# Kernel tuning notes

Hardware: AMD Instinct MI355X
Metric: run time of the kernel (lower is better)

Reference implementation:

```python
import jax, jax.numpy as jnp
from jax import lax
import numpy as np

B, S, D, H = 8, 1024, 512, 8
DH, FF, INNER, K = D // H, 4 * D, 2 * D, 31
SQRT_D = float(np.sqrt(D))  # module scales by sqrt(dim), not sqrt(dim_head)


def _ln(x, g, b, eps=1e-5):
    m = jnp.mean(x, -1, keepdims=True)
    v = jnp.var(x, -1, keepdims=True)
    return (x - m) / jnp.sqrt(v + eps) * g + b


def _swish(x):
    return x * jax.nn.sigmoid(x)


def _ff(x, g, b, w1, b1, w2, b2):
    return _swish(_ln(x, g, b) @ w1 + b1) @ w2 + b2


def _pos_encoding(s, d):
    pos = jnp.arange(s, dtype=jnp.float32)[:, None]
    div = jnp.exp(jnp.arange(0, d, 2, dtype=jnp.float32) * (-np.log(10000.0) / d))
    pe = jnp.zeros((s, d), jnp.float32)
    pe = pe.at[:, 0::2].set(jnp.sin(pos * div))
    pe = pe.at[:, 1::2].set(jnp.cos(pos * div))
    return pe


def _rel_shift(ps):  # (b, h, s, t) Transformer-XL relative shift
    b, h, s, t = ps.shape
    ps = jnp.pad(ps, ((0, 0), (0, 0), (0, 0), (1, 0)))
    return ps.reshape(b, h, t + 1, s)[:, :, 1:].reshape(b, h, s, t)


def _forward(x, ff1_ln_g, ff1_ln_b, ff1_w1, ff1_b1, ff1_w2, ff1_b2,
             attn_ln_g, attn_ln_b, wq, bq, wk, bk, wv, bv, wpos,
             u_bias, v_bias, wo, bo,
             conv_ln_g, conv_ln_b, pw1_w, pw1_b, dw_w, dw_b,
             bn_g, bn_b, bn_mean, bn_var, pw2_w, pw2_b,
             ff2_ln_g, ff2_ln_b, ff2_w1, ff2_b1, ff2_w2, ff2_b2,
             norm_g, norm_b):
    b, s, d = x.shape
    # FF1 half-residual
    x = 0.5 * _ff(x, ff1_ln_g, ff1_ln_b, ff1_w1, ff1_b1, ff1_w2, ff1_b2) + x
    # relative-position multi-head self-attention
    y = _ln(x, attn_ln_g, attn_ln_b)
    q = (y @ wq + bq).reshape(b, s, H, DH)
    k = (y @ wk + bk).reshape(b, s, H, DH)
    v = (y @ wv + bv).reshape(b, s, H, DH)
    pos = (_pos_encoding(s, d) @ wpos).reshape(s, H, DH)  # identical across batch
    score = jnp.einsum('bshd,bthd->bhst', q + u_bias, k)
    pos_score = _rel_shift(jnp.einsum('bshd,thd->bhst', q + v_bias, pos))
    attn = jax.nn.softmax((score + pos_score) / SQRT_D, axis=-1)
    ctx = jnp.einsum('bhst,bthd->bshd', attn, v).reshape(b, s, d)
    x = ctx @ wo + bo + x
    # conformer conv module: LN -> pointwise -> GLU -> depthwise -> BN -> swish -> pointwise
    c = _ln(x, conv_ln_g, conv_ln_b) @ pw1_w + pw1_b  # (b, s, 2*inner)
    a, gate = jnp.split(c, 2, axis=-1)
    z = jnp.transpose(a * jax.nn.sigmoid(gate), (0, 2, 1))  # (b, inner, s)
    z = jnp.pad(z, ((0, 0), (0, 0), (K // 2, K // 2)))  # pad (15, 15) for k=31
    z = lax.conv_general_dilated(z, dw_w[:, None, :], (1,), 'VALID',
                                 dimension_numbers=('NCH', 'OIH', 'NCH'),
                                 feature_group_count=INNER) + dw_b[None, :, None]
    z = (z - bn_mean[None, :, None]) * (bn_g / jnp.sqrt(bn_var + 1e-5))[None, :, None] + bn_b[None, :, None]
    z = _swish(z)
    x = jnp.transpose(z, (0, 2, 1)) @ pw2_w + pw2_b + x
    # FF2 half-residual + final LN
    x = 0.5 * _ff(x, ff2_ln_g, ff2_ln_b, ff2_w1, ff2_b1, ff2_w2, ff2_b2) + x
    return _ln(x, norm_g, norm_b)


def setup_inputs() -> dict:
    key = jax.random.key(0)
    ks = iter(jax.random.split(key, 64))

    def w(shape, scale=0.02):
        return scale * jax.random.normal(next(ks), shape, jnp.float32)

    return {
        'x': jax.random.normal(next(ks), (B, S, D), jnp.float32),
        'ff1_ln_g': jnp.ones(D, jnp.float32), 'ff1_ln_b': jnp.zeros(D, jnp.float32),
        'ff1_w1': w((D, FF)), 'ff1_b1': jnp.zeros(FF, jnp.float32),
        'ff1_w2': w((FF, D)), 'ff1_b2': jnp.zeros(D, jnp.float32),
        'attn_ln_g': jnp.ones(D, jnp.float32), 'attn_ln_b': jnp.zeros(D, jnp.float32),
        'wq': w((D, D)), 'bq': jnp.zeros(D, jnp.float32),
        'wk': w((D, D)), 'bk': jnp.zeros(D, jnp.float32),
        'wv': w((D, D)), 'bv': jnp.zeros(D, jnp.float32),
        'wpos': w((D, D)),
        'u_bias': w((H, DH)), 'v_bias': w((H, DH)),
        'wo': w((D, D)), 'bo': jnp.zeros(D, jnp.float32),
        'conv_ln_g': jnp.ones(D, jnp.float32), 'conv_ln_b': jnp.zeros(D, jnp.float32),
        'pw1_w': w((D, 2 * INNER)), 'pw1_b': jnp.zeros(2 * INNER, jnp.float32),
        'dw_w': w((INNER, K)), 'dw_b': jnp.zeros(INNER, jnp.float32),
        'bn_g': jnp.ones(INNER, jnp.float32), 'bn_b': jnp.zeros(INNER, jnp.float32),
        'bn_mean': jnp.zeros(INNER, jnp.float32), 'bn_var': jnp.ones(INNER, jnp.float32),
        'pw2_w': w((INNER, D)), 'pw2_b': jnp.zeros(D, jnp.float32),
        'ff2_ln_g': jnp.ones(D, jnp.float32), 'ff2_ln_b': jnp.zeros(D, jnp.float32),
        'ff2_w1': w((D, FF)), 'ff2_b1': jnp.zeros(FF, jnp.float32),
        'ff2_w2': w((FF, D)), 'ff2_b2': jnp.zeros(D, jnp.float32),
        'norm_g': jnp.ones(D, jnp.float32), 'norm_b': jnp.zeros(D, jnp.float32),
    }


def reference(x, ff1_ln_g, ff1_ln_b, ff1_w1, ff1_b1, ff1_w2, ff1_b2,
              attn_ln_g, attn_ln_b, wq, bq, wk, bk, wv, bv, wpos,
              u_bias, v_bias, wo, bo,
              conv_ln_g, conv_ln_b, pw1_w, pw1_b, dw_w, dw_b,
              bn_g, bn_b, bn_mean, bn_var, pw2_w, pw2_b,
              ff2_ln_g, ff2_ln_b, ff2_w1, ff2_b1, ff2_w2, ff2_b2,
              norm_g, norm_b):
    return _forward(x, ff1_ln_g, ff1_ln_b, ff1_w1, ff1_b1, ff1_w2, ff1_b2,
                    attn_ln_g, attn_ln_b, wq, bq, wk, bk, wv, bv, wpos,
                    u_bias, v_bias, wo, bo,
                    conv_ln_g, conv_ln_b, pw1_w, pw1_b, dw_w, dw_b,
                    bn_g, bn_b, bn_mean, bn_var, pw2_w, pw2_b,
                    ff2_ln_g, ff2_ln_b, ff2_w1, ff2_b1, ff2_w2, ff2_b2,
                    norm_g, norm_b)
```

## Files before the change

kernel.cpp:

```cpp
#include <hip/hip_runtime.h>
#include <cstdint>
#include <cstddef>

#define B_ 8
#define S_ 1024
#define D_ 512
#define H_ 8
#define DH_ 64
#define FF_ 2048
#define INNER_ 1024
#define NROWS 8192
#define INV_SQRT_D 0.04419417382415922f

typedef __attribute__((ext_vector_type(8))) short bf16x8;
typedef __attribute__((ext_vector_type(4))) float f32x4;
struct alignas(8) short4x { short x, y, z, w; };

__device__ __forceinline__ float sigmoidf_(float x) { return 1.f / (1.f + expf(-x)); }

__device__ __forceinline__ short f2bf(float f) {
  uint32_t u = __float_as_uint(f);
  u += 0x7fff + ((u >> 16) & 1);
  return (short)(u >> 16);
}
__device__ __forceinline__ float bf2f(short s) {
  return __uint_as_float(((uint32_t)(uint16_t)s) << 16);
}

__device__ __forceinline__ void store_out(float* C, size_t i, float v) { C[i] = v; }
__device__ __forceinline__ void store_out(short* C, size_t i, float v) { C[i] = f2bf(v); }

__device__ __forceinline__ void gload_lds16(const void* g, void* lds) {
  __builtin_amdgcn_global_load_lds(
      (const __attribute__((address_space(1))) uint32_t*)g,
      (__attribute__((address_space(3))) uint32_t*)lds, 16, 0, 0);
}

template <typename OutT>
__global__ __launch_bounds__(256) void ln_kernel(const float* __restrict__ in,
    const float* __restrict__ g, const float* __restrict__ b,
    OutT* __restrict__ out) {
  int row = blockIdx.x;
  const float* x = in + (size_t)row * D_;
  OutT* o = out + (size_t)row * D_;
  int t = threadIdx.x;
  float v0 = x[t], v1 = x[t + 256];
  float s = v0 + v1, q = v0 * v0 + v1 * v1;
#pragma unroll
  for (int off = 32; off > 0; off >>= 1) {
    s += __shfl_down(s, off);
    q += __shfl_down(q, off);
  }
  __shared__ float red[8];
  int wid = t >> 6, lane = t & 63;
  if (lane == 0) { red[wid] = s; red[wid + 4] = q; }
  __syncthreads();
  if (t == 0) {
    float S = red[0] + red[1] + red[2] + red[3];
    float Q = red[4] + red[5] + red[6] + red[7];
    float mean = S * (1.f / D_);
    float var = Q * (1.f / D_) - mean * mean;
    red[0] = mean;
    red[1] = rsqrtf(var + 1e-5f);
  }
  __syncthreads();
  float mean = red[0], inv = red[1];
  store_out(o, t, (v0 - mean) * inv * g[t] + b[t]);
  store_out(o, t + 256, (v1 - mean) * inv * g[t + 256] + b[t + 256]);
}

__global__ __launch_bounds__(256) void transpose_bf16_kernel(const float* __restrict__ in,
    short* __restrict__ out, int K, int N) {
  __shared__ float t[32][33];
  int n0 = blockIdx.x << 5, k0 = blockIdx.y << 5;
  int tx = threadIdx.x & 31, ty = threadIdx.x >> 5;
#pragma unroll
  for (int e = 0; e < 4; ++e)
    t[ty + e * 8][tx] = in[(size_t)(k0 + ty + e * 8) * N + n0 + tx];
  __syncthreads();
#pragma unroll
  for (int e = 0; e < 4; ++e)
    out[(size_t)(n0 + ty + e * 8) * K + k0 + tx] = f2bf(t[tx][ty + e * 8]);
}

template <int EPI, typename OutT>
__global__ __launch_bounds__(256) void mfma_gemm(const short* __restrict__ A,
    const short* __restrict__ Bt, const float* __restrict__ bias,
    const float* __restrict__ res, OutT* __restrict__ C, short* __restrict__ C2,
    const float* __restrict__ bias2, const float* __restrict__ bias3,
    int M, int N, int K) {
  __shared__ short As[128 * 32];
  __shared__ short Bs[128 * 32];
  int tid = threadIdx.x;
  int w = tid >> 6, l = tid & 63;
  int nwg = gridDim.x * gridDim.y;
  int flat = blockIdx.y * gridDim.x + blockIdx.x;
  int W = (flat & 7) * (nwg >> 3) + (flat >> 3);
  int bm = (W / gridDim.x) << 7, bn = (W % gridDim.x) << 7;
  int wr = w >> 1, wc = w & 1;
  f32x4 acc[4][4] = {};

  int sr = l >> 2, sc = l & 3;
  int r0 = (w * 2 + 0) * 16 + sr;
  int r1 = (w * 2 + 1) * 16 + sr;
  int g0 = sc ^ ((r0 >> 1) & 3);
  int g1 = sc ^ ((r1 >> 1) & 3);
  const short* a0 = A + (size_t)(bm + r0) * K + g0 * 8;
  const short* a1 = A + (size_t)(bm + r1) * K + g1 * 8;
  const short* b0 = Bt + (size_t)(bn + r0) * K + g0 * 8;
  const short* b1 = Bt + (size_t)(bn + r1) * K + g1 * 8;
  short* asd0 = As + (w * 2 + 0) * 512;
  short* asd1 = As + (w * 2 + 1) * 512;
  short* bsd0 = Bs + (w * 2 + 0) * 512;
  short* bsd1 = Bs + (w * 2 + 1) * 512;

  int lcol = l & 15, lk = l >> 4;
  int aoff[4], boff[4];
#pragma unroll
  for (int m = 0; m < 4; ++m) {
    int r = wr * 64 + m * 16 + lcol;
    aoff[m] = r * 32 + ((lk ^ ((r >> 1) & 3)) << 3);
  }
#pragma unroll
  for (int n = 0; n < 4; ++n) {
    int r = wc * 64 + n * 16 + lcol;
    boff[n] = r * 32 + ((lk ^ ((r >> 1) & 3)) << 3);
  }

  for (int k0 = 0; k0 < K; k0 += 32) {
    gload_lds16(a0 + k0, asd0);
    gload_lds16(a1 + k0, asd1);
    gload_lds16(b0 + k0, bsd0);
    gload_lds16(b1 + k0, bsd1);
    __syncthreads();
    bf16x8 af[4], bfr[4];
#pragma unroll
    for (int m = 0; m < 4; ++m) af[m] = *(const bf16x8*)(As + aoff[m]);
#pragma unroll
    for (int n = 0; n < 4; ++n) bfr[n] = *(const bf16x8*)(Bs + boff[n]);
#pragma unroll
    for (int m = 0; m < 4; ++m)
#pragma unroll
      for (int n = 0; n < 4; ++n)
        acc[m][n] = __builtin_amdgcn_mfma_f32_16x16x32_bf16(af[m], bfr[n], acc[m][n], 0, 0, 0);
    __syncthreads();
  }

  int lrow = (l >> 4) << 2;
#pragma unroll
  for (int m = 0; m < 4; ++m) {
    int row0 = bm + wr * 64 + m * 16 + lrow;
#pragma unroll
    for (int n = 0; n < 4; ++n) {
      int col = bn + wc * 64 + n * 16 + lcol;
      float bv = bias ? bias[col] : 0.f;
      if (EPI == 5) {
        short4x o;
        o.x = f2bf(acc[m][n][0] + bv);
        o.y = f2bf(acc[m][n][1] + bv);
        o.z = f2bf(acc[m][n][2] + bv);
        o.w = f2bf(acc[m][n][3] + bv);
        size_t tidx = ((size_t)(row0 >> 10) * 512 + col) * 1024 + (row0 & 1023);
        *(short4x*)((short*)C + tidx) = o;
      } else if (EPI == 4) {
#pragma unroll
        for (int r = 0; r < 4; ++r) {
          size_t idx = (size_t)(row0 + r) * N + col;
          float v = acc[m][n][r] + bv;
          ((short*)C)[idx] = f2bf(v + bias2[col]);
          C2[idx] = f2bf(v + bias3[col]);
        }
      } else {
#pragma unroll
        for (int r = 0; r < 4; ++r) {
          size_t idx = (size_t)(row0 + r) * N + col;
          float v = acc[m][n][r] + bv;
          if (EPI == 1) v = v * sigmoidf_(v);
          else if (EPI == 2) v = 0.5f * v + res[idx];
          else if (EPI == 3) v = v + res[idx];
          store_out(C, idx, v);
        }
      }
    }
  }
}

__global__ __launch_bounds__(256) void pe_kernel(short* __restrict__ pe) {
  int t = blockIdx.x, i = threadIdx.x;
  float freq = expf((float)(2 * i) * (-9.2103403719761836f / 512.f));
  float arg = (float)t * freq;
  pe[(size_t)t * D_ + 2 * i] = f2bf(sinf(arg));
  pe[(size_t)t * D_ + 2 * i + 1] = f2bf(cosf(arg));
}

__global__ __launch_bounds__(256) void attn_pos_mfma(const short* __restrict__ Qb,
    const short* __restrict__ Pos, short* __restrict__ Out, int bh0) {
  __shared__ short Qs[128 * 64];
  __shared__ short Ks[128 * 64];
  int tid = threadIdx.x;
  int w = tid >> 6, l = tid & 63;
  int z = blockIdx.z;
  int bh = bh0 + z, b = bh >> 3, h = bh & 7;
  int bi = blockIdx.y << 7, bj = blockIdx.x << 7;
  int srow = w * 8 + (l >> 3);
  int sch = l & 7;
#pragma unroll
  for (int cc = 0; cc < 4; ++cc) {
    int r = cc * 32 + srow;
    int g = sch ^ (r & 7);
    gload_lds16(Qb + (size_t)(b * S_ + bi + r) * D_ + h * DH_ + g * 8, Qs + (cc * 32 + w * 8) * 64);
    gload_lds16(Pos + (size_t)(bj + r) * D_ + h * DH_ + g * 8, Ks + (cc * 32 + w * 8) * 64);
  }
  __syncthreads();
  int wr = w >> 1, wc = w & 1;
  int lcol = l & 15, lk = l >> 4;
  bf16x8 qf[4][2], kf[4][2];
#pragma unroll
  for (int m = 0; m < 4; ++m)
#pragma unroll
    for (int ks = 0; ks < 2; ++ks) {
      int r = wr * 64 + m * 16 + lcol;
      int c = ks * 4 + lk;
      qf[m][ks] = *(const bf16x8*)(Qs + r * 64 + ((c ^ (r & 7)) << 3));
    }
#pragma unroll
  for (int n = 0; n < 4; ++n)
#pragma unroll
    for (int ks = 0; ks < 2; ++ks) {
      int r = wc * 64 + n * 16 + lcol;
      int c = ks * 4 + lk;
      kf[n][ks] = *(const bf16x8*)(Ks + r * 64 + ((c ^ (r & 7)) << 3));
    }
  f32x4 acc[4][4] = {};
#pragma unroll
  for (int ks = 0; ks < 2; ++ks)
#pragma unroll
    for (int m = 0; m < 4; ++m)
#pragma unroll
      for (int n = 0; n < 4; ++n)
        acc[m][n] = __builtin_amdgcn_mfma_f32_16x16x32_bf16(qf[m][ks], kf[n][ks], acc[m][n], 0, 0, 0);
  int lrow = (l >> 4) << 2;
  short* Oz = Out + (size_t)z * S_ * S_;
#pragma unroll
  for (int m = 0; m < 4; ++m)
#pragma unroll
    for (int r = 0; r < 4; ++r) {
      int iG = bi + wr * 64 + m * 16 + lrow + r;
#pragma unroll
      for (int n = 0; n < 4; ++n) {
        int tG = bj + wc * 64 + n * 16 + lcol;
        short val = f2bf(acc[m][n][r]);
        if (tG >= S_ - 1 - iG)
          Oz[(size_t)iG * S_ + (tG - (S_ - 1 - iG))] = val;
        else if (iG >= 1)
          Oz[(size_t)(iG - 1) * S_ + (tG + iG + 1)] = val;
        if (tG == 0 && iG < S_ - 1)
          Oz[(size_t)iG * S_ + iG + 1] = 0;
      }
    }
}

__global__ __launch_bounds__(512) void attn_fused(const short* __restrict__ qu,
    const short* __restrict__ kk, const short* __restrict__ vT,
    const short* __restrict__ Psh, short* __restrict__ ctx, int bh0) {
  __shared__ short Ks[2][64 * 64];
  __shared__ short Vs[2][64 * 64];
  __shared__ short Ps[128 * 64];
  int tid = threadIdx.x;
  int w = tid >> 6, l = tid & 63;
  int z = blockIdx.y;
  int bh = bh0 + z, b = bh >> 3, h = bh & 7;
  int i0 = blockIdx.x << 7;
  bf16x8 qf0, qf1;
  {
    const short* qrow = qu + (size_t)(b * S_ + i0 + w * 16 + (l & 15)) * D_ + h * DH_ + ((l >> 4) << 3);
    qf0 = *(const bf16x8*)(qrow);
    qf1 = *(const bf16x8*)(qrow + 32);
  }
  f32x4 po[4] = {};
  float mrow[4], lrw[4];
  int gi[4];
#pragma unroll
  for (int r = 0; r < 4; ++r) {
    mrow[r] = -1e30f;
    lrw[r] = 0.f;
    gi[r] = i0 + w * 16 + ((l >> 4) << 2) + r;
  }
  const short* prow0 = Psh + (size_t)z * S_ * S_ + (size_t)gi[0] * S_ + (l & 15);
  const short* prow1 = prow0 + S_;
  const short* prow2 = prow1 + S_;
  const short* prow3 = prow2 + S_;

  int srw = (w << 3) + (l >> 3);
  int sg = (l & 7) ^ (srw & 7);
  const short* ksrc = kk + (size_t)(b * S_) * D_ + h * DH_ + (sg << 3);
  const short* vsrc = vT + (size_t)(b * 512 + h * DH_ + srw) * 1024 + (sg << 3);
  int sdst = (w << 3) * 64;

#define STAGE_KV(jt, buf)                                                  \
  {                                                                        \
    int j0_ = (jt) << 6;                                                   \
    gload_lds16(ksrc + (size_t)(j0_ + srw) * D_, &Ks[buf][sdst]);          \
    gload_lds16(vsrc + j0_, &Vs[buf][sdst]);                               \
  }

  float pvc[4][4], pvn[4][4];
#define PLOADF(jt, dst)                                                    \
  {                                                                        \
    int j0_ = (jt) << 6;                                                   \
    _Pragma("unroll") for (int n_ = 0; n_ < 4; ++n_) {                     \
      dst[n_][0] = bf2f(prow0[j0_ + (n_ << 4)]);                           \
      dst[n_][1] = bf2f(prow1[j0_ + (n_ << 4)]);                           \
      dst[n_][2] = bf2f(prow2[j0_ + (n_ << 4)]);                           \
      dst[n_][3] = bf2f(prow3[j0_ + (n_ << 4)]);                           \
    }                                                                      \
  }

  STAGE_KV(0, 0);
  PLOADF(0, pvc);
  __syncthreads();

  for (int jt = 0; jt < 16; ++jt) {
    int buf = jt & 1;
    if (jt < 15) {
      STAGE_KV(jt + 1, buf ^ 1);
      PLOADF(jt + 1, pvn);
    }
    f32x4 sc[4] = {};
#pragma unroll
    for (int ks = 0; ks < 2; ++ks)
#pragma unroll
      for (int n = 0; n < 4; ++n) {
        int rj = (n << 4) + (l & 15);
        int ck = (ks << 2) + (l >> 4);
        bf16x8 kf = *(const bf16x8*)(&Ks[buf][rj * 64 + ((ck ^ (rj & 7)) << 3)]);
        sc[n] = __builtin_amdgcn_mfma_f32_16x16x32_bf16(ks == 0 ? qf0 : qf1, kf, sc[n], 0, 0, 0);
      }
    float pm[4];
#pragma unroll
    for (int r = 0; r < 4; ++r) pm[r] = -1e30f;
#pragma unroll
    for (int n = 0; n < 4; ++n)
#pragma unroll
      for (int r = 0; r < 4; ++r) {
        float v = (sc[n][r] + pvc[n][r]) * INV_SQRT_D;
        sc[n][r] = v;
        pm[r] = fmaxf(pm[r], v);
      }
#pragma unroll
    for (int r = 0; r < 4; ++r)
#pragma unroll
      for (int off = 1; off < 16; off <<= 1) pm[r] = fmaxf(pm[r], __shfl_xor(pm[r], off));
    float psum[4];
#pragma unroll
    for (int r = 0; r < 4; ++r) {
      float mn = fmaxf(mrow[r], pm[r]);
      float f = __expf(mrow[r] - mn);
      mrow[r] = mn;
      lrw[r] *= f;
#pragma unroll
      for (int n = 0; n < 4; ++n) po[n][r] *= f;
      psum[r] = 0.f;
    }
#pragma unroll
    for (int n = 0; n < 4; ++n)
#pragma unroll
      for (int r = 0; r < 4; ++r) {
        float p = __expf(sc[n][r] - mrow[r]);
        psum[r] += p;
        int rr = (w << 4) + ((l >> 4) << 2) + r;
        int c = (n << 4) + (l & 15);
        Ps[rr * 64 + (((c >> 3) ^ (rr & 7)) << 3) + (c & 7)] = f2bf(p);
      }
#pragma unroll
    for (int r = 0; r < 4; ++r) {
#pragma unroll
      for (int off = 1; off < 16; off <<= 1) psum[r] += __shfl_xor(psum[r], off);
      lrw[r] += psum[r];
    }
    int rr2 = (w << 4) + (l & 15);
    bf16x8 pa[2];
#pragma unroll
    for (int ks = 0; ks < 2; ++ks) {
      int ck = (ks << 2) + (l >> 4);
      pa[ks] = *(const bf16x8*)(&Ps[rr2 * 64 + ((ck ^ (rr2 & 7)) << 3)]);
    }
#pragma unroll
    for (int ks = 0; ks < 2; ++ks)
#pragma unroll
      for (int n = 0; n < 4; ++n) {
        int rd = (n << 4) + (l & 15);
        int ck = (ks << 2) + (l >> 4);
        bf16x8 vf = *(const bf16x8*)(&Vs[buf][rd * 64 + ((ck ^ (rd & 7)) << 3)]);
        po[n] = __builtin_amdgcn_mfma_f32_16x16x32_bf16(pa[ks], vf, po[n], 0, 0, 0);
      }
    __syncthreads();
    if (jt < 15) {
#pragma unroll
      for (int n = 0; n < 4; ++n)
#pragma unroll
        for (int r = 0; r < 4; ++r) pvc[n][r] = pvn[n][r];
    }
  }
  short* Cz = ctx + (size_t)b * S_ * D_ + h * DH_;
#pragma unroll
  for (int r = 0; r < 4; ++r) {
    float inv = 1.f / lrw[r];
#pragma unroll
    for (int n = 0; n < 4; ++n)
      Cz[(size_t)gi[r] * D_ + (n << 4) + (l & 15)] = f2bf(po[n][r] * inv);
  }
#undef STAGE_KV
#undef PLOADF
}

__global__ __launch_bounds__(256) void glu_kernel(const short* __restrict__ hbuf,
                                                  short* __restrict__ z) {
  size_t idx4 = ((size_t)blockIdx.x * 256 + threadIdx.x) << 2;
  size_t row = idx4 >> 10, c = idx4 & 1023;
  short4x a4 = *(const short4x*)(hbuf + row * 2048 + c);
  short4x g4 = *(const short4x*)(hbuf + row * 2048 + 1024 + c);
  short4x o;
  o.x = f2bf(bf2f(a4.x) * sigmoidf_(bf2f(g4.x)));
  o.y = f2bf(bf2f(a4.y) * sigmoidf_(bf2f(g4.y)));
  o.z = f2bf(bf2f(a4.z) * sigmoidf_(bf2f(g4.z)));
  o.w = f2bf(bf2f(a4.w) * sigmoidf_(bf2f(g4.w)));
  *(short4x*)(z + idx4) = o;
}

#define CTS 32
__global__ __launch_bounds__(256) void dwconv_kernel(const short* __restrict__ z,
    const float* __restrict__ w, const float* __restrict__ wb,
    const float* __restrict__ bng, const float* __restrict__ bnb,
    const float* __restrict__ bnm, const float* __restrict__ bnv,
    short* __restrict__ out) {
  int c = (blockIdx.z << 8) + threadIdx.x;
  int b = blockIdx.y;
  int s0 = blockIdx.x * CTS;
  float wr[31];
#pragma unroll
  for (int kk = 0; kk < 31; ++kk) wr[kk] = w[c * 31 + kk];
  float zv[CTS + 30];
#pragma unroll
  for (int e = 0; e < CTS + 30; ++e) {
    int sr = s0 - 15 + e;
    zv[e] = (sr >= 0 && sr < S_) ? bf2f(z[((size_t)(b * S_ + sr) << 10) + c]) : 0.f;
  }
  float scale = bng[c] * rsqrtf(bnv[c] + 1e-5f);
  float shift = bnb[c] - bnm[c] * scale;
  float bias = wb[c];
#pragma unroll
  for (int s = 0; s < CTS; ++s) {
    float acc = 0.f;
#pragma unroll
    for (int kk = 0; kk < 31; ++kk) acc += zv[s + kk] * wr[kk];
    float v = (acc + bias) * scale + shift;
    v = v * sigmoidf_(v);
    out[((size_t)(b * S_ + s0 + s) << 10) + c] = f2bf(v);
  }
}

extern "C" void kernel_launch(void* const* d_in, const int* in_sizes, int n_in,
                              void* d_out, int out_size, void* d_ws, size_t ws_size,
                              hipStream_t stream) {
  const float* x_in = (const float*)d_in[0];
  const float* ff1_ln_g = (const float*)d_in[1];
  const float* ff1_ln_b = (const float*)d_in[2];
  const float* ff1_w1 = (const float*)d_in[3];
  const float* ff1_b1 = (const float*)d_in[4];
  const float* ff1_w2 = (const float*)d_in[5];
  const float* ff1_b2 = (const float*)d_in[6];
  const float* attn_ln_g = (const float*)d_in[7];
  const float* attn_ln_b = (const float*)d_in[8];
  const float* wq = (const float*)d_in[9];
  const float* bq = (const float*)d_in[10];
  const float* wk = (const float*)d_in[11];
  const float* bk = (const float*)d_in[12];
  const float* wv = (const float*)d_in[13];
  const float* bv = (const float*)d_in[14];
  const float* wpos = (const float*)d_in[15];
  const float* u_bias = (const float*)d_in[16];
  const float* v_bias = (const float*)d_in[17];
  const float* wo = (const float*)d_in[18];
  const float* bo = (const float*)d_in[19];
  const float* conv_ln_g = (const float*)d_in[20];
  const float* conv_ln_b = (const float*)d_in[21];
  const float* pw1_w = (const float*)d_in[22];
  const float* pw1_b = (const float*)d_in[23];
  const float* dw_w = (const float*)d_in[24];
  const float* dw_b = (const float*)d_in[25];
  const float* bn_g = (const float*)d_in[26];
  const float* bn_b = (const float*)d_in[27];
  const float* bn_mean = (const float*)d_in[28];
  const float* bn_var = (const float*)d_in[29];
  const float* pw2_w = (const float*)d_in[30];
  const float* pw2_b = (const float*)d_in[31];
  const float* ff2_ln_g = (const float*)d_in[32];
  const float* ff2_ln_b = (const float*)d_in[33];
  const float* ff2_w1 = (const float*)d_in[34];
  const float* ff2_b1 = (const float*)d_in[35];
  const float* ff2_w2 = (const float*)d_in[36];
  const float* ff2_b2 = (const float*)d_in[37];
  const float* norm_g = (const float*)d_in[38];
  const float* norm_b = (const float*)d_in[39];

  char* wsb = (char*)d_ws;
  float* xb = (float*)(wsb);
  short* yb16 = (short*)(wsb + (16ull << 20));
  short* qu16 = (short*)(wsb + (24ull << 20));
  short* qv16 = (short*)(wsb + (32ull << 20));
  short* k16 = (short*)(wsb + (40ull << 20));
  short* vT16 = (short*)(wsb + (48ull << 20));
  short* ctx16 = (short*)(wsb + (56ull << 20));
  short* pos16 = (short*)(wsb + (64ull << 20));
  short* wt = (short*)(wsb + (65ull << 20));
  short* Pb16 = (short*)(wsb + (80ull << 20));
  short* hb16 = (short*)(wsb + (80ull << 20));
  short* zb16 = (short*)(wsb + (112ull << 20));
  short* cb16 = (short*)(wsb + (128ull << 20));
  short* peb16 = ctx16;

  short* ff1w1t = wt;
  short* ff1w2t = ff1w1t + 2048 * 512;
  short* wqt = ff1w2t + 512 * 2048;
  short* wkt = wqt + 512 * 512;
  short* wvt = wkt + 512 * 512;
  short* wot = wvt + 512 * 512;
  short* wpost = wot + 512 * 512;
  short* pw1t = wpost + 512 * 512;
  short* pw2t = pw1t + 2048 * 512;
  short* ff2w1t = pw2t + 512 * 1024;
  short* ff2w2t = ff2w1t + 2048 * 512;

  dim3 blk(256);

  transpose_bf16_kernel<<<dim3(64, 16), blk, 0, stream>>>(ff1_w1, ff1w1t, 512, 2048);
  transpose_bf16_kernel<<<dim3(16, 64), blk, 0, stream>>>(ff1_w2, ff1w2t, 2048, 512);
  transpose_bf16_kernel<<<dim3(16, 16), blk, 0, stream>>>(wq, wqt, 512, 512);
  transpose_bf16_kernel<<<dim3(16, 16), blk, 0, stream>>>(wk, wkt, 512, 512);
  transpose_bf16_kernel<<<dim3(16, 16), blk, 0, stream>>>(wv, wvt, 512, 512);
  transpose_bf16_kernel<<<dim3(16, 16), blk, 0, stream>>>(wo, wot, 512, 512);
  transpose_bf16_kernel<<<dim3(16, 16), blk, 0, stream>>>(wpos, wpost, 512, 512);
  transpose_bf16_kernel<<<dim3(64, 16), blk, 0, stream>>>(pw1_w, pw1t, 512, 2048);
  transpose_bf16_kernel<<<dim3(16, 32), blk, 0, stream>>>(pw2_w, pw2t, 1024, 512);
  transpose_bf16_kernel<<<dim3(64, 16), blk, 0, stream>>>(ff2_w1, ff2w1t, 512, 2048);
  transpose_bf16_kernel<<<dim3(16, 64), blk, 0, stream>>>(ff2_w2, ff2w2t, 2048, 512);

  ln_kernel<short><<<NROWS, blk, 0, stream>>>(x_in, ff1_ln_g, ff1_ln_b, yb16);
  mfma_gemm<1, short><<<dim3(FF_ / 128, NROWS / 128), blk, 0, stream>>>(yb16, ff1w1t, ff1_b1, nullptr, hb16, nullptr, nullptr, nullptr, NROWS, FF_, D_);
  mfma_gemm<2, float><<<dim3(D_ / 128, NROWS / 128), blk, 0, stream>>>(hb16, ff1w2t, ff1_b2, x_in, xb, nullptr, nullptr, nullptr, NROWS, D_, FF_);

  ln_kernel<short><<<NROWS, blk, 0, stream>>>(xb, attn_ln_g, attn_ln_b, yb16);
  mfma_gemm<4, short><<<dim3(D_ / 128, NROWS / 128), blk, 0, stream>>>(yb16, wqt, bq, nullptr, qu16, qv16, u_bias, v_bias, NROWS, D_, D_);
  mfma_gemm<0, short><<<dim3(D_ / 128, NROWS / 128), blk, 0, stream>>>(yb16, wkt, bk, nullptr, k16, nullptr, nullptr, nullptr, NROWS, D_, D_);
  mfma_gemm<5, short><<<dim3(D_ / 128, NROWS / 128), blk, 0, stream>>>(yb16, wvt, bv, nullptr, vT16, nullptr, nullptr, nullptr, NROWS, D_, D_);
  pe_kernel<<<S_, blk, 0, stream>>>(peb16);
  mfma_gemm<0, short><<<dim3(D_ / 128, S_ / 128), blk, 0, stream>>>(peb16, wpost, nullptr, nullptr, pos16, nullptr, nullptr, nullptr, S_, D_, D_);

  const int CH = 32;
  for (int c = 0; c < 64 / CH; ++c) {
    int bh0 = c * CH;
    attn_pos_mfma<<<dim3(8, 8, CH), blk, 0, stream>>>(qv16, pos16, Pb16, bh0);
    attn_fused<<<dim3(S_ / 128, CH), dim3(512), 0, stream>>>(qu16, k16, vT16, Pb16, ctx16, bh0);
  }
  mfma_gemm<3, float><<<dim3(D_ / 128, NROWS / 128), blk, 0, stream>>>(ctx16, wot, bo, xb, xb, nullptr, nullptr, nullptr, NROWS, D_, D_);

  ln_kernel<short><<<NROWS, blk, 0, stream>>>(xb, conv_ln_g, conv_ln_b, yb16);
  mfma_gemm<0, short><<<dim3(2 * INNER_ / 128, NROWS / 128), blk, 0, stream>>>(yb16, pw1t, pw1_b, nullptr, hb16, nullptr, nullptr, nullptr, NROWS, 2 * INNER_, D_);
  glu_kernel<<<NROWS * INNER_ / 1024, blk, 0, stream>>>(hb16, zb16);
  dwconv_kernel<<<dim3(S_ / CTS, B_, 4), blk, 0, stream>>>(zb16, dw_w, dw_b, bn_g, bn_b, bn_mean, bn_var, cb16);
  mfma_gemm<3, float><<<dim3(D_ / 128, NROWS / 128), blk, 0, stream>>>(cb16, pw2t, pw2_b, xb, xb, nullptr, nullptr, nullptr, NROWS, D_, INNER_);

  ln_kernel<short><<<NROWS, blk, 0, stream>>>(xb, ff2_ln_g, ff2_ln_b, yb16);
  mfma_gemm<1, short><<<dim3(FF_ / 128, NROWS / 128), blk, 0, stream>>>(yb16, ff2w1t, ff2_b1, nullptr, hb16, nullptr, nullptr, nullptr, NROWS, FF_, D_);
  mfma_gemm<2, float><<<dim3(D_ / 128, NROWS / 128), blk, 0, stream>>>(hb16, ff2w2t, ff2_b2, xb, xb, nullptr, nullptr, nullptr, NROWS, D_, FF_);

  ln_kernel<float><<<NROWS, blk, 0, stream>>>(xb, norm_g, norm_b, (float*)d_out);
}
```

Measured before the change: 571.5 us.

## Double-buffer LDS in MFMA GEMM and use 128x64 tiles for N=512 GEMMs

Adds a ping-pong LDS buffer to the GEMM so the next K-tile's global-to-LDS loads are issued before the current tile's MFMAs, leaving one barrier per iteration instead of two. It also templates the GEMM on the N tile width and uses 64-wide tiles for every N=512 GEMM, doubling their workgroup count (from 256 to 512 for the 8192-row ones) to fill more CUs. The cost is more LDS per block and less operand reuse per tile for those GEMMs.

```diff
diff --git a/kernel.cpp b/kernel.cpp
--- a/kernel.cpp
+++ b/kernel.cpp
@@ -83,65 +83,77 @@
     out[(size_t)(n0 + ty + e * 8) * K + k0 + tx] = f2bf(t[tx][ty + e * 8]);
 }
 
-template <int EPI, typename OutT>
+template <int BN, int EPI, typename OutT>
 __global__ __launch_bounds__(256) void mfma_gemm(const short* __restrict__ A,
     const short* __restrict__ Bt, const float* __restrict__ bias,
     const float* __restrict__ res, OutT* __restrict__ C, short* __restrict__ C2,
     const float* __restrict__ bias2, const float* __restrict__ bias3,
     int M, int N, int K) {
-  __shared__ short As[128 * 32];
-  __shared__ short Bs[128 * 32];
+  constexpr int NFN = BN / 32;
+  __shared__ short As[2][128 * 32];
+  __shared__ short Bs[2][BN * 32];
   int tid = threadIdx.x;
   int w = tid >> 6, l = tid & 63;
   int nwg = gridDim.x * gridDim.y;
   int flat = blockIdx.y * gridDim.x + blockIdx.x;
   int W = (flat & 7) * (nwg >> 3) + (flat >> 3);
-  int bm = (W / gridDim.x) << 7, bn = (W % gridDim.x) << 7;
+  int bm = (W / gridDim.x) << 7, bn = (W % gridDim.x) * BN;
   int wr = w >> 1, wc = w & 1;
-  f32x4 acc[4][4] = {};
+  f32x4 acc[4][NFN] = {};
 
   int sr = l >> 2, sc = l & 3;
-  int r0 = (w * 2 + 0) * 16 + sr;
-  int r1 = (w * 2 + 1) * 16 + sr;
-  int g0 = sc ^ ((r0 >> 1) & 3);
-  int g1 = sc ^ ((r1 >> 1) & 3);
-  const short* a0 = A + (size_t)(bm + r0) * K + g0 * 8;
-  const short* a1 = A + (size_t)(bm + r1) * K + g1 * 8;
-  const short* b0 = Bt + (size_t)(bn + r0) * K + g0 * 8;
-  const short* b1 = Bt + (size_t)(bn + r1) * K + g1 * 8;
-  short* asd0 = As + (w * 2 + 0) * 512;
-  short* asd1 = As + (w * 2 + 1) * 512;
-  short* bsd0 = Bs + (w * 2 + 0) * 512;
-  short* bsd1 = Bs + (w * 2 + 1) * 512;
+  int ra0 = (w * 2 + 0) * 16 + sr;
+  int ra1 = (w * 2 + 1) * 16 + sr;
+  int ga0 = sc ^ ((ra0 >> 1) & 3);
+  int ga1 = sc ^ ((ra1 >> 1) & 3);
+  const short* a0 = A + (size_t)(bm + ra0) * K + ga0 * 8;
+  const short* a1 = A + (size_t)(bm + ra1) * K + ga1 * 8;
+  int rb0 = (BN == 128) ? ra0 : (w * 16 + sr);
+  int gb0 = sc ^ ((rb0 >> 1) & 3);
+  const short* b0 = Bt + (size_t)(bn + rb0) * K + gb0 * 8;
+  const short* b1 = Bt + (size_t)(bn + ra1) * K + ga1 * 8;
+  int asd0 = (w * 2 + 0) * 512;
+  int asd1 = (w * 2 + 1) * 512;
+  int bsd0 = (BN == 128) ? asd0 : w * 512;
 
   int lcol = l & 15, lk = l >> 4;
-  int aoff[4], boff[4];
+  int aoff[4], boff[NFN];
 #pragma unroll
   for (int m = 0; m < 4; ++m) {
     int r = wr * 64 + m * 16 + lcol;
     aoff[m] = r * 32 + ((lk ^ ((r >> 1) & 3)) << 3);
   }
 #pragma unroll
-  for (int n = 0; n < 4; ++n) {
-    int r = wc * 64 + n * 16 + lcol;
+  for (int n = 0; n < NFN; ++n) {
+    int r = wc * (BN / 2) + n * 16 + lcol;
     boff[n] = r * 32 + ((lk ^ ((r >> 1) & 3)) << 3);
   }
 
-  for (int k0 = 0; k0 < K; k0 += 32) {
-    gload_lds16(a0 + k0, asd0);
-    gload_lds16(a1 + k0, asd1);
-    gload_lds16(b0 + k0, bsd0);
-    gload_lds16(b1 + k0, bsd1);
-    __syncthreads();
-    bf16x8 af[4], bfr[4];
-#pragma unroll
-    for (int m = 0; m < 4; ++m) af[m] = *(const bf16x8*)(As + aoff[m]);
-#pragma unroll
-    for (int n = 0; n < 4; ++n) bfr[n] = *(const bf16x8*)(Bs + boff[n]);
+  int nt = K >> 5;
+  gload_lds16(a0, &As[0][asd0]);
+  gload_lds16(a1, &As[0][asd1]);
+  gload_lds16(b0, &Bs[0][bsd0]);
+  if constexpr (BN == 128) gload_lds16(b1, &Bs[0][asd1]);
+  __syncthreads();
+
+  for (int t = 0; t < nt; ++t) {
+    int cur = t & 1;
+    if (t + 1 < nt) {
+      int k1 = (t + 1) << 5;
+      gload_lds16(a0 + k1, &As[cur ^ 1][asd0]);
+      gload_lds16(a1 + k1, &As[cur ^ 1][asd1]);
+      gload_lds16(b0 + k1, &Bs[cur ^ 1][bsd0]);
+      if constexpr (BN == 128) gload_lds16(b1 + k1, &Bs[cur ^ 1][asd1]);
+    }
+    bf16x8 af[4], bfr[NFN];
+#pragma unroll
+    for (int m = 0; m < 4; ++m) af[m] = *(const bf16x8*)(&As[cur][aoff[m]]);
+#pragma unroll
+    for (int n = 0; n < NFN; ++n) bfr[n] = *(const bf16x8*)(&Bs[cur][boff[n]]);
 #pragma unroll
     for (int m = 0; m < 4; ++m)
 #pragma unroll
-      for (int n = 0; n < 4; ++n)
+      for (int n = 0; n < NFN; ++n)
         acc[m][n] = __builtin_amdgcn_mfma_f32_16x16x32_bf16(af[m], bfr[n], acc[m][n], 0, 0, 0);
     __syncthreads();
   }
@@ -151,8 +163,8 @@
   for (int m = 0; m < 4; ++m) {
     int row0 = bm + wr * 64 + m * 16 + lrow;
 #pragma unroll
-    for (int n = 0; n < 4; ++n) {
-      int col = bn + wc * 64 + n * 16 + lcol;
+    for (int n = 0; n < NFN; ++n) {
+      int col = bn + wc * (BN / 2) + n * 16 + lcol;
       float bv = bias ? bias[col] : 0.f;
       if (EPI == 5) {
         short4x o;
@@ -547,15 +559,15 @@
   transpose_bf16_kernel<<<dim3(16, 64), blk, 0, stream>>>(ff2_w2, ff2w2t, 2048, 512);
 
   ln_kernel<short><<<NROWS, blk, 0, stream>>>(x_in, ff1_ln_g, ff1_ln_b, yb16);
-  mfma_gemm<1, short><<<dim3(FF_ / 128, NROWS / 128), blk, 0, stream>>>(yb16, ff1w1t, ff1_b1, nullptr, hb16, nullptr, nullptr, nullptr, NROWS, FF_, D_);
-  mfma_gemm<2, float><<<dim3(D_ / 128, NROWS / 128), blk, 0, stream>>>(hb16, ff1w2t, ff1_b2, x_in, xb, nullptr, nullptr, nullptr, NROWS, D_, FF_);
+  mfma_gemm<128, 1, short><<<dim3(FF_ / 128, NROWS / 128), blk, 0, stream>>>(yb16, ff1w1t, ff1_b1, nullptr, hb16, nullptr, nullptr, nullptr, NROWS, FF_, D_);
+  mfma_gemm<64, 2, float><<<dim3(D_ / 64, NROWS / 128), blk, 0, stream>>>(hb16, ff1w2t, ff1_b2, x_in, xb, nullptr, nullptr, nullptr, NROWS, D_, FF_);
 
   ln_kernel<short><<<NROWS, blk, 0, stream>>>(xb, attn_ln_g, attn_ln_b, yb16);
-  mfma_gemm<4, short><<<dim3(D_ / 128, NROWS / 128), blk, 0, stream>>>(yb16, wqt, bq, nullptr, qu16, qv16, u_bias, v_bias, NROWS, D_, D_);
-  mfma_gemm<0, short><<<dim3(D_ / 128, NROWS / 128), blk, 0, stream>>>(yb16, wkt, bk, nullptr, k16, nullptr, nullptr, nullptr, NROWS, D_, D_);
-  mfma_gemm<5, short><<<dim3(D_ / 128, NROWS / 128), blk, 0, stream>>>(yb16, wvt, bv, nullptr, vT16, nullptr, nullptr, nullptr, NROWS, D_, D_);
+  mfma_gemm<64, 4, short><<<dim3(D_ / 64, NROWS / 128), blk, 0, stream>>>(yb16, wqt, bq, nullptr, qu16, qv16, u_bias, v_bias, NROWS, D_, D_);
+  mfma_gemm<64, 0, short><<<dim3(D_ / 64, NROWS / 128), blk, 0, stream>>>(yb16, wkt, bk, nullptr, k16, nullptr, nullptr, nullptr, NROWS, D_, D_);
+  mfma_gemm<64, 5, short><<<dim3(D_ / 64, NROWS / 128), blk, 0, stream>>>(yb16, wvt, bv, nullptr, vT16, nullptr, nullptr, nullptr, NROWS, D_, D_);
   pe_kernel<<<S_, blk, 0, stream>>>(peb16);
-  mfma_gemm<0, short><<<dim3(D_ / 128, S_ / 128), blk, 0, stream>>>(peb16, wpost, nullptr, nullptr, pos16, nullptr, nullptr, nullptr, S_, D_, D_);
+  mfma_gemm<64, 0, short><<<dim3(D_ / 64, S_ / 128), blk, 0, stream>>>(peb16, wpost, nullptr, nullptr, pos16, nullptr, nullptr, nullptr, S_, D_, D_);
 
   const int CH = 32;
   for (int c = 0; c < 64 / CH; ++c) {
@@ -563,17 +575,17 @@
     attn_pos_mfma<<<dim3(8, 8, CH), blk, 0, stream>>>(qv16, pos16, Pb16, bh0);
     attn_fused<<<dim3(S_ / 128, CH), dim3(512), 0, stream>>>(qu16, k16, vT16, Pb16, ctx16, bh0);
   }
-  mfma_gemm<3, float><<<dim3(D_ / 128, NROWS / 128), blk, 0, stream>>>(ctx16, wot, bo, xb, xb, nullptr, nullptr, nullptr, NROWS, D_, D_);
+  mfma_gemm<64, 3, float><<<dim3(D_ / 64, NROWS / 128), blk, 0, stream>>>(ctx16, wot, bo, xb, xb, nullptr, nullptr, nullptr, NROWS, D_, D_);
 
   ln_kernel<short><<<NROWS, blk, 0, stream>>>(xb, conv_ln_g, conv_ln_b, yb16);
-  mfma_gemm<0, short><<<dim3(2 * INNER_ / 128, NROWS / 128), blk, 0, stream>>>(yb16, pw1t, pw1_b, nullptr, hb16, nullptr, nullptr, nullptr, NROWS, 2 * INNER_, D_);
+  mfma_gemm<128, 0, short><<<dim3(2 * INNER_ / 128, NROWS / 128), blk, 0, stream>>>(yb16, pw1t, pw1_b, nullptr, hb16, nullptr, nullptr, nullptr, NROWS, 2 * INNER_, D_);
   glu_kernel<<<NROWS * INNER_ / 1024, blk, 0, stream>>>(hb16, zb16);
   dwconv_kernel<<<dim3(S_ / CTS, B_, 4), blk, 0, stream>>>(zb16, dw_w, dw_b, bn_g, bn_b, bn_mean, bn_var, cb16);
-  mfma_gemm<3, float><<<dim3(D_ / 128, NROWS / 128), blk, 0, stream>>>(cb16, pw2t, pw2_b, xb, xb, nullptr, nullptr, nullptr, NROWS, D_, INNER_);
+  mfma_gemm<64, 3, float><<<dim3(D_ / 64, NROWS / 128), blk, 0, stream>>>(cb16, pw2t, pw2_b, xb, xb, nullptr, nullptr, nullptr, NROWS, D_, INNER_);
 
   ln_kernel<short><<<NROWS, blk, 0, stream>>>(xb, ff2_ln_g, ff2_ln_b, yb16);
-  mfma_gemm<1, short><<<dim3(FF_ / 128, NROWS / 128), blk, 0, stream>>>(yb16, ff2w1t, ff2_b1, nullptr, hb16, nullptr, nullptr, nullptr, NROWS, FF_, D_);
-  mfma_gemm<2, float><<<dim3(D_ / 128, NROWS / 128), blk, 0, stream>>>(hb16, ff2w2t, ff2_b2, xb, xb, nullptr, nullptr, nullptr, NROWS, D_, FF_);
+  mfma_gemm<128, 1, short><<<dim3(FF_ / 128, NROWS / 128), blk, 0, stream>>>(yb16, ff2w1t, ff2_b1, nullptr, hb16, nullptr, nullptr, nullptr, NROWS, FF_, D_);
+  mfma_gemm<64, 2, float><<<dim3(D_ / 64, NROWS / 128), blk, 0, stream>>>(hb16, ff2w2t, ff2_b2, xb, xb, nullptr, nullptr, nullptr, NROWS, D_, FF_);
 
   ln_kernel<float><<<NROWS, blk, 0, stream>>>(xb, norm_g, norm_b, (float*)d_out);
 }
```

After: 512.2 us. -10.4%, faster.
